# Kernel optimization log

Measured on AMD Instinct MI355X. Metric: run time of the kernel, lower is better.

## Reference

```python
import jax, jax.numpy as jnp
import numpy as np

N_NODES = 50000
N_EDGES = 640000
N_REL = 8
IN_DIM = 128
HID_DIM = 128
OUT_DIM = 64


def setup_inputs() -> dict:
    key = jax.random.key(0)
    ks = jax.random.split(key, 8)
    features = jax.random.normal(ks[0], (N_NODES, IN_DIM), dtype=jnp.float32)
    src = jax.random.randint(ks[1], (N_EDGES,), 0, N_NODES, dtype=jnp.int32)
    dst = jax.random.randint(ks[2], (N_EDGES,), 0, N_NODES, dtype=jnp.int32)
    edge_types = jax.random.randint(ks[3], (N_EDGES,), 0, N_REL, dtype=jnp.int32)
    s1 = 1.0 / np.sqrt(IN_DIM)
    s2 = 1.0 / np.sqrt(HID_DIM)
    W1 = jax.random.normal(ks[4], (N_REL, IN_DIM, HID_DIM), dtype=jnp.float32) * s1
    W1_self = jax.random.normal(ks[5], (IN_DIM, HID_DIM), dtype=jnp.float32) * s1
    b1 = jnp.zeros((HID_DIM,), dtype=jnp.float32)
    W2 = jax.random.normal(ks[6], (N_REL, HID_DIM, OUT_DIM), dtype=jnp.float32) * s2
    W2_self = jax.random.normal(ks[7], (HID_DIM, OUT_DIM), dtype=jnp.float32) * s2
    b2 = jnp.zeros((OUT_DIM,), dtype=jnp.float32)
    return {"features": features, "src": src, "dst": dst, "edge_types": edge_types,
            "W1": W1, "W1_self": W1_self, "b1": b1,
            "W2": W2, "W2_self": W2_self, "b2": b2}


def _rel_graph_conv(h, src, dst, edge_types, W, W_self, b):
    # Precompute relation-specific transforms for all nodes: [R, N, Dout]
    rel = jnp.einsum('nd,rdo->rno', h, W)
    # Gather per-edge message W[etype(e)] @ h[src(e)]: [E, Dout]
    msg = rel[edge_types, src]
    # Scatter-sum to destination nodes
    agg = jax.ops.segment_sum(msg, dst, num_segments=h.shape[0])
    # Self-loop + bias (DGL RelGraphConv defaults: self_loop=True, bias=True)
    return agg + h @ W_self + b


def reference(features, src, dst, edge_types, W1, W1_self, b1, W2, W2_self, b2):
    h = jax.nn.relu(_rel_graph_conv(features, src, dst, edge_types, W1, W1_self, b1))
    logits = _rel_graph_conv(h, src, dst, edge_types, W2, W2_self, b2)
    return logits
```

## Files before the change

kernel.cpp:

```cpp
#include <hip/hip_runtime.h>
#include <hip/hip_bf16.h>
#include <stdint.h>

#define NN 50000
#define NE 640000
#define NR 8
#define NK (NR * NN)
#define NPB 391

typedef short bf16x8 __attribute__((ext_vector_type(8)));
typedef float f32x4  __attribute__((ext_vector_type(4)));

__device__ __forceinline__ unsigned short f2bf(float f) {
    union { float f; unsigned u; } v; v.f = f;
    unsigned r = v.u + 0x7FFF + ((v.u >> 16) & 1);
    return (unsigned short)(r >> 16);
}

__global__ __launch_bounds__(256) void prep0_kernel(
        const float* __restrict__ X,
        const float* __restrict__ W1, const float* __restrict__ W1s,
        const float* __restrict__ W2, const float* __restrict__ W2s,
        unsigned short* __restrict__ Xbf,
        unsigned short* __restrict__ W1T, unsigned short* __restrict__ W2T,
        int* __restrict__ counts) {
    const int gid = blockIdx.x * 256 + threadIdx.x;
    const int gsz = gridDim.x * 256;

    for (int i = gid; i < NK / 4; i += gsz)
        ((uint4*)counts)[i] = make_uint4(0, 0, 0, 0);

    for (int i = gid; i < NN * 16; i += gsz) {
        const float4* pp = (const float4*)X + (size_t)i * 2;
        float4 a = pp[0], b = pp[1];
        uint4 o;
        o.x = (unsigned)f2bf(a.x) | ((unsigned)f2bf(a.y) << 16);
        o.y = (unsigned)f2bf(a.z) | ((unsigned)f2bf(a.w) << 16);
        o.z = (unsigned)f2bf(b.x) | ((unsigned)f2bf(b.y) << 16);
        o.w = (unsigned)f2bf(b.z) | ((unsigned)f2bf(b.w) << 16);
        ((uint4*)Xbf)[i] = o;
    }

    for (int i = gid; i < 9 * 128 * 128; i += gsz) {
        int k = i & 127, c = i >> 7;
        int r = c >> 7, o = c & 127;
        float v = (r < 8) ? W1[((size_t)r * 128 + k) * 128 + o]
                          : W1s[(size_t)k * 128 + o];
        W1T[i] = f2bf(v);
    }

    for (int i = gid; i < 9 * 64 * 128; i += gsz) {
        int k = i & 127, c = i >> 7;
        int r = c >> 6, o = c & 63;
        float v = (r < 8) ? W2[((size_t)r * 128 + k) * 64 + o]
                          : W2s[(size_t)k * 64 + o];
        W2T[i] = f2bf(v);
    }
}

__global__ void hist2_kernel(const int* __restrict__ dst, const int* __restrict__ et,
                             int* __restrict__ counts) {
    int e = blockIdx.x * 256 + threadIdx.x;
    if (e < NE) atomicAdd(&counts[et[e] * NN + dst[e]], 1);
}

__global__ __launch_bounds__(1024) void blocksum_kernel(const int* __restrict__ counts,
                                                        int* __restrict__ bsum, int n) {
    __shared__ int ws[16];
    int i = blockIdx.x * 1024 + threadIdx.x;
    int v = (i < n) ? counts[i] : 0;
    #pragma unroll
    for (int d = 32; d > 0; d >>= 1) v += __shfl_down(v, d, 64);
    int wid = threadIdx.x >> 6, lane = threadIdx.x & 63;
    if (lane == 0) ws[wid] = v;
    __syncthreads();
    if (threadIdx.x < 16) {
        int s = ws[threadIdx.x];
        #pragma unroll
        for (int d = 8; d > 0; d >>= 1) s += __shfl_down(s, d, 16);
        if (threadIdx.x == 0) bsum[blockIdx.x] = s;
    }
}

__global__ __launch_bounds__(1024) void scanlocal2_kernel(const int* __restrict__ counts,
                                                          const int* __restrict__ bsum,
                                                          int* __restrict__ offsets,
                                                          int* __restrict__ cursor, int n) {
    __shared__ int ws[16];
    __shared__ int wbase[16];
    __shared__ int base_sh;
    const int t = threadIdx.x, b = blockIdx.x;
    const int i = b * 1024 + t;
    const int lane = t & 63, wid = t >> 6;

    int v = (i < n) ? counts[i] : 0;
    int incl = v;
    #pragma unroll
    for (int d = 1; d < 64; d <<= 1) {
        int nv = __shfl_up(incl, d, 64);
        if (lane >= d) incl += nv;
    }
    if (lane == 63) ws[wid] = incl;
    __syncthreads();
    if (t < 16) {
        int s = ws[t], si = s;
        #pragma unroll
        for (int d = 1; d < 16; d <<= 1) {
            int nv = __shfl_up(si, d, 16);
            if (t >= d) si += nv;
        }
        wbase[t] = si - s;
    }
    __syncthreads();
    int local_excl = wbase[wid] + incl - v;

    if (wid == 0) {
        int acc = 0;
        for (int j = lane; j < b; j += 64) acc += bsum[j];
        #pragma unroll
        for (int d = 32; d > 0; d >>= 1) acc += __shfl_down(acc, d, 64);
        if (lane == 0) base_sh = acc;
    }
    __syncthreads();

    if (i < n) {
        int excl = base_sh + local_excl;
        offsets[i] = excl;
        cursor[i]  = excl;
    }
    if (b == 0 && t == 0) offsets[NK] = NE;
}

__global__ void fill2_kernel(const int* __restrict__ src, const int* __restrict__ dst,
                             const int* __restrict__ et, int* __restrict__ cursor,
                             int* __restrict__ esrc) {
    int e = blockIdx.x * 256 + threadIdx.x;
    if (e < NE) {
        int pos = atomicAdd(&cursor[et[e] * NN + dst[e]], 1);
        esrc[pos] = src[e];
    }
}

template<int NOUT, bool RELU, bool OUTBF16>
__global__ __launch_bounds__(256) void fused_layer(
        const unsigned short* __restrict__ A,
        const unsigned short* __restrict__ WT,
        const float* __restrict__ bias,
        const int* __restrict__ off2,
        const int* __restrict__ esrc,
        void* __restrict__ outp, int M) {
    constexpr int CW = NOUT / 4;
    constexpr int NJ = CW / 16;
    __shared__ unsigned short Asw[64 * 128];

    const int t = threadIdx.x;
    const int n0 = blockIdx.x * 64;
    const int bm = (M - n0 < 64) ? (M - n0) : 64;
    const int lane = t & 63;
    const int w = t >> 6;
    const int r15 = lane & 15;
    const int q = lane >> 4;

    const int key = t >> 2;
    const int sub = t & 3;
    const int kk = n0 + key;
    const bool kv = (kk < M);

    f32x4 acc[4][NJ] = {};

    auto do_mfma = [&](int rr) {
        #pragma unroll
        for (int ks = 0; ks < 4; ks++) {
            int c = (ks * 4 + q) ^ r15;
            bf16x8 af[4];
            #pragma unroll
            for (int i = 0; i < 4; i++)
                af[i] = *(const bf16x8*)((const char*)Asw + (i * 16 + r15) * 256 + (c << 4));
            #pragma unroll
            for (int j = 0; j < NJ; j++) {
                bf16x8 bf = *(const bf16x8*)(WT +
                    ((size_t)(rr * NOUT + w * CW + j * 16 + r15) << 7) + ks * 32 + q * 8);
                #pragma unroll
                for (int i = 0; i < 4; i++)
                    acc[i][j] = __builtin_amdgcn_mfma_f32_16x16x32_bf16(af[i], bf, acc[i][j], 0, 0, 0);
            }
        }
    };

    int e0 = kv ? off2[kk] : 0;
    int e1 = kv ? off2[kk + 1] : 0;

    #pragma unroll
    for (int kc = 0; kc < 4; kc++) {
        int g = t + kc * 256;
        int row = g >> 4, c = g & 15;
        uint4 v = make_uint4(0, 0, 0, 0);
        if (row < bm) v = *(const uint4*)(A + ((size_t)(n0 + row) << 7) + c * 8);
        *(uint4*)((char*)Asw + row * 256 + ((c ^ (row & 15)) << 4)) = v;
    }
    __syncthreads();
    do_mfma(8);

    for (int r = 0; r < 8; r++) {
        int e0n = 0, e1n = 0;
        if (r < 7 && kv) {
            e0n = off2[(r + 1) * NN + kk];
            e1n = off2[(r + 1) * NN + kk + 1];
        }

        float a[32];
        #pragma unroll
        for (int i = 0; i < 32; i++) a[i] = 0.f;
        for (int e = e0; e < e1; ++e) {
            int s = esrc[e];
            const uint4* rp = (const uint4*)((const unsigned*)A + ((size_t)s << 6) + sub * 16);
            #pragma unroll
            for (int u4 = 0; u4 < 4; ++u4) {
                uint4 v = rp[u4];
                unsigned uu[4] = {v.x, v.y, v.z, v.w};
                #pragma unroll
                for (int j = 0; j < 4; ++j) {
                    a[u4 * 8 + j * 2 + 0] += __uint_as_float(uu[j] << 16);
                    a[u4 * 8 + j * 2 + 1] += __uint_as_float(uu[j] & 0xffff0000u);
                }
            }
        }
        __syncthreads();

        #pragma unroll
        for (int c4 = 0; c4 < 4; ++c4) {
            uint4 pv;
            pv.x = (unsigned)f2bf(a[c4 * 8 + 0]) | ((unsigned)f2bf(a[c4 * 8 + 1]) << 16);
            pv.y = (unsigned)f2bf(a[c4 * 8 + 2]) | ((unsigned)f2bf(a[c4 * 8 + 3]) << 16);
            pv.z = (unsigned)f2bf(a[c4 * 8 + 4]) | ((unsigned)f2bf(a[c4 * 8 + 5]) << 16);
            pv.w = (unsigned)f2bf(a[c4 * 8 + 6]) | ((unsigned)f2bf(a[c4 * 8 + 7]) << 16);
            int c = sub * 4 + c4;
            *(uint4*)((char*)Asw + key * 256 + ((c ^ (key & 15)) << 4)) = pv;
        }
        __syncthreads();

        do_mfma(r);
        e0 = e0n; e1 = e1n;
    }

    #pragma unroll
    for (int j = 0; j < NJ; j++) {
        int col = w * CW + j * 16 + r15;
        float bv = bias[col];
        #pragma unroll
        for (int i = 0; i < 4; i++) {
            #pragma unroll
            for (int reg = 0; reg < 4; reg++) {
                int m = n0 + i * 16 + q * 4 + reg;
                if (m < M) {
                    float v = acc[i][j][reg] + bv;
                    if (RELU) v = fmaxf(v, 0.f);
                    if (OUTBF16)
                        ((unsigned short*)outp)[(size_t)m * NOUT + col] = f2bf(v);
                    else
                        ((float*)outp)[(size_t)m * NOUT + col] = v;
                }
            }
        }
    }
}

extern "C" void kernel_launch(void* const* d_in, const int* in_sizes, int n_in,
                              void* d_out, int out_size, void* d_ws, size_t ws_size,
                              hipStream_t stream) {
    const float* X   = (const float*)d_in[0];
    const int*   src = (const int*)d_in[1];
    const int*   dst = (const int*)d_in[2];
    const int*   et  = (const int*)d_in[3];
    const float* W1  = (const float*)d_in[4];
    const float* W1s = (const float*)d_in[5];
    const float* b1  = (const float*)d_in[6];
    const float* W2  = (const float*)d_in[7];
    const float* W2s = (const float*)d_in[8];
    const float* b2  = (const float*)d_in[9];
    float* out = (float*)d_out;

    char* p = (char*)d_ws;
    unsigned short* Xbf = (unsigned short*)p; p += (size_t)NN * 128 * 2;
    unsigned short* hbf = (unsigned short*)p; p += (size_t)NN * 128 * 2;
    unsigned short* W1T = (unsigned short*)p; p += (size_t)9 * 128 * 128 * 2;
    unsigned short* W2T = (unsigned short*)p; p += (size_t)9 * 64 * 128 * 2;
    int* counts2 = (int*)p; p += (size_t)NK * 4;
    int* off2    = (int*)p; p += (size_t)(NK + 4) * 4;
    int* cursor2 = (int*)p; p += (size_t)NK * 4;
    int* esrc    = (int*)p; p += (size_t)NE * 4;
    int* bsum    = (int*)p; p += 512 * 4;
    int* bbase   = (int*)p; p += 512 * 4;

    prep0_kernel<<<2048, 256, 0, stream>>>(X, W1, W1s, W2, W2s, Xbf, W1T, W2T, counts2);
    hist2_kernel<<<(NE + 255) / 256, 256, 0, stream>>>(dst, et, counts2);
    blocksum_kernel<<<NPB, 1024, 0, stream>>>(counts2, bsum, NK);
    scanlocal2_kernel<<<NPB, 1024, 0, stream>>>(counts2, bsum, off2, cursor2, NK);
    fill2_kernel<<<(NE + 255) / 256, 256, 0, stream>>>(src, dst, et, cursor2, esrc);

    const int nblk = (NN + 63) / 64;

    fused_layer<128, true, true><<<nblk, 256, 0, stream>>>(
        Xbf, W1T, b1, off2, esrc, hbf, NN);
    fused_layer<64, false, false><<<nblk, 256, 0, stream>>>(
        hbf, W2T, b2, off2, esrc, out, NN);
}
```

Before: 297.0 us.

## Fuse histogram into prep kernel and merge block-sum into scan

Zeroing of the counts array moves to a memset, and the edge histogram atomics run inside the prep kernel, so one launch disappears. The separate block-sum kernel is removed: each scan block now sums all preceding counts itself to get its base offset. This cuts launches and inter-kernel syncs, but later blocks re-read up to 400K counts, which adds quadratic redundant reads across the grid.

```diff
diff --git a/kernel.cpp b/kernel.cpp
--- a/kernel.cpp
+++ b/kernel.cpp
@@ -21,14 +21,15 @@
         const float* __restrict__ X,
         const float* __restrict__ W1, const float* __restrict__ W1s,
         const float* __restrict__ W2, const float* __restrict__ W2s,
+        const int* __restrict__ dst, const int* __restrict__ et,
         unsigned short* __restrict__ Xbf,
         unsigned short* __restrict__ W1T, unsigned short* __restrict__ W2T,
         int* __restrict__ counts) {
     const int gid = blockIdx.x * 256 + threadIdx.x;
     const int gsz = gridDim.x * 256;
 
-    for (int i = gid; i < NK / 4; i += gsz)
-        ((uint4*)counts)[i] = make_uint4(0, 0, 0, 0);
+    for (int e = gid; e < NE; e += gsz)
+        atomicAdd(&counts[et[e] * NN + dst[e]], 1);
 
     for (int i = gid; i < NN * 16; i += gsz) {
         const float4* pp = (const float4*)X + (size_t)i * 2;
@@ -58,41 +59,23 @@
     }
 }
 
-__global__ void hist2_kernel(const int* __restrict__ dst, const int* __restrict__ et,
-                             int* __restrict__ counts) {
-    int e = blockIdx.x * 256 + threadIdx.x;
-    if (e < NE) atomicAdd(&counts[et[e] * NN + dst[e]], 1);
-}
-
-__global__ __launch_bounds__(1024) void blocksum_kernel(const int* __restrict__ counts,
-                                                        int* __restrict__ bsum, int n) {
-    __shared__ int ws[16];
-    int i = blockIdx.x * 1024 + threadIdx.x;
-    int v = (i < n) ? counts[i] : 0;
-    #pragma unroll
-    for (int d = 32; d > 0; d >>= 1) v += __shfl_down(v, d, 64);
-    int wid = threadIdx.x >> 6, lane = threadIdx.x & 63;
-    if (lane == 0) ws[wid] = v;
-    __syncthreads();
-    if (threadIdx.x < 16) {
-        int s = ws[threadIdx.x];
-        #pragma unroll
-        for (int d = 8; d > 0; d >>= 1) s += __shfl_down(s, d, 16);
-        if (threadIdx.x == 0) bsum[blockIdx.x] = s;
-    }
-}
-
-__global__ __launch_bounds__(1024) void scanlocal2_kernel(const int* __restrict__ counts,
-                                                          const int* __restrict__ bsum,
-                                                          int* __restrict__ offsets,
-                                                          int* __restrict__ cursor, int n) {
+__global__ __launch_bounds__(1024) void scanfused_kernel(const int* __restrict__ counts,
+                                                         int* __restrict__ offsets,
+                                                         int* __restrict__ cursor, int n) {
     __shared__ int ws[16];
     __shared__ int wbase[16];
+    __shared__ int wsum[16];
     __shared__ int base_sh;
     const int t = threadIdx.x, b = blockIdx.x;
     const int i = b * 1024 + t;
     const int lane = t & 63, wid = t >> 6;
 
+    int acc = 0;
+    for (int j = t; j < b * 1024; j += 1024) acc += counts[j];
+    #pragma unroll
+    for (int d = 32; d > 0; d >>= 1) acc += __shfl_down(acc, d, 64);
+    if (lane == 0) wsum[wid] = acc;
+
     int v = (i < n) ? counts[i] : 0;
     int incl = v;
     #pragma unroll
@@ -111,20 +94,16 @@
         }
         wbase[t] = si - s;
     }
+    if (t == 16) {
+        int s = 0;
+        #pragma unroll
+        for (int j = 0; j < 16; j++) s += wsum[j];
+        base_sh = s;
+    }
     __syncthreads();
-    int local_excl = wbase[wid] + incl - v;
-
-    if (wid == 0) {
-        int acc = 0;
-        for (int j = lane; j < b; j += 64) acc += bsum[j];
-        #pragma unroll
-        for (int d = 32; d > 0; d >>= 1) acc += __shfl_down(acc, d, 64);
-        if (lane == 0) base_sh = acc;
-    }
-    __syncthreads();
 
     if (i < n) {
-        int excl = base_sh + local_excl;
+        int excl = base_sh + wbase[wid] + incl - v;
         offsets[i] = excl;
         cursor[i]  = excl;
     }
@@ -292,10 +271,10 @@
     int* bsum    = (int*)p; p += 512 * 4;
     int* bbase   = (int*)p; p += 512 * 4;
 
-    prep0_kernel<<<2048, 256, 0, stream>>>(X, W1, W1s, W2, W2s, Xbf, W1T, W2T, counts2);
-    hist2_kernel<<<(NE + 255) / 256, 256, 0, stream>>>(dst, et, counts2);
-    blocksum_kernel<<<NPB, 1024, 0, stream>>>(counts2, bsum, NK);
-    scanlocal2_kernel<<<NPB, 1024, 0, stream>>>(counts2, bsum, off2, cursor2, NK);
+    hipMemsetAsync(counts2, 0, (size_t)NK * sizeof(int), stream);
+    prep0_kernel<<<2048, 256, 0, stream>>>(X, W1, W1s, W2, W2s, dst, et,
+                                           Xbf, W1T, W2T, counts2);
+    scanfused_kernel<<<NPB, 1024, 0, stream>>>(counts2, off2, cursor2, NK);
     fill2_kernel<<<(NE + 255) / 256, 256, 0, stream>>>(src, dst, et, cursor2, esrc);
 
     const int nblk = (NN + 63) / 64;
```

After: 334.9 us. 12.8% more time.
